# Optimization experiments

Measured on AMD Instinct MI355X. Metric: run time of the kernel, lower is better.

Reference implementation:

```python
import jax, jax.numpy as jnp
import numpy as np

T, B, S = 32, 128, 64          # decode steps, batch, source length
H = 1024                        # hidden size
EW, EF = 512, 64                # word / field embedding sizes
VW, VF = 32000, 512             # word / field vocab sizes
L = 2                           # GRU layers


def setup_inputs() -> dict:
    key = jax.random.key(0)
    ks = jax.random.split(key, 24)
    s = 0.02
    return {
        "word_ids": jax.random.randint(ks[0], (T, B), 0, VW),
        "field_ids": jax.random.randint(ks[1], (T, B), 0, VF),
        "lengths": jnp.full((B,), S, dtype=jnp.int32),  # unused in forward math
        "hidden": jax.random.normal(ks[2], (L, B, H), jnp.float32) * s,
        "context": jax.random.normal(ks[3], (B, S, H), jnp.float32),
        "context_mask": jnp.ones((B, S), dtype=bool),
        "prev_output": jnp.zeros((B, H), jnp.float32),
        "word_emb_table": jax.random.normal(ks[4], (VW, EW), jnp.float32) * s,
        "field_emb_table": jax.random.normal(ks[5], (VF, EF), jnp.float32) * s,
        "gru0_Wih": jax.random.normal(ks[6], (3 * H, EW + EF + H), jnp.float32) * s,
        "gru0_Whh": jax.random.normal(ks[7], (3 * H, H), jnp.float32) * s,
        "gru0_bih": jnp.zeros((3 * H,), jnp.float32),
        "gru0_bhh": jnp.zeros((3 * H,), jnp.float32),
        "gru1_Wih": jax.random.normal(ks[8], (3 * H, H), jnp.float32) * s,
        "gru1_Whh": jax.random.normal(ks[9], (3 * H, H), jnp.float32) * s,
        "gru1_bih": jnp.zeros((3 * H,), jnp.float32),
        "gru1_bhh": jnp.zeros((3 * H,), jnp.float32),
        "attn_Wa": jax.random.normal(ks[10], (H, H), jnp.float32) * s,
        "attn_Wc": jax.random.normal(ks[11], (H, 2 * H), jnp.float32) * s,
        "gen_Ww": jax.random.normal(ks[12], (VW, H), jnp.float32) * s,
        "gen_bw": jnp.zeros((VW,), jnp.float32),
        "gen_Wf": jax.random.normal(ks[13], (VF, H), jnp.float32) * s,
        "gen_bf": jnp.zeros((VF,), jnp.float32),
    }


def _gru_cell(x, h, Wih, Whh, bih, bhh):
    # torch.nn.GRUCell math
    gi = x @ Wih.T + bih      # (B, 3H)
    gh = h @ Whh.T + bhh
    i_r, i_z, i_n = jnp.split(gi, 3, axis=-1)
    h_r, h_z, h_n = jnp.split(gh, 3, axis=-1)
    r = jax.nn.sigmoid(i_r + h_r)
    z = jax.nn.sigmoid(i_z + h_z)
    n = jnp.tanh(i_n + r * h_n)
    return (1.0 - z) * n + z * h


def _forward(word_ids, field_ids, hidden, context, context_mask, prev_output,
             word_emb_table, field_emb_table,
             gru0_Wih, gru0_Whh, gru0_bih, gru0_bhh,
             gru1_Wih, gru1_Whh, gru1_bih, gru1_bhh,
             attn_Wa, attn_Wc, gen_Ww, gen_bw, gen_Wf, gen_bf):
    w_emb = jnp.take(word_emb_table, word_ids, axis=0)    # (T, B, EW)
    f_emb = jnp.take(field_emb_table, field_ids, axis=0)  # (T, B, EF)

    def step(carry, emb):
        hid, out = carry
        we, fe = emb
        x = jnp.concatenate([we, fe, out], axis=-1)        # input feeding
        h0 = _gru_cell(x, hid[0], gru0_Wih, gru0_Whh, gru0_bih, gru0_bhh)
        h1 = _gru_cell(h0, hid[1], gru1_Wih, gru1_Whh, gru1_bih, gru1_bhh)
        new_hid = jnp.stack([h0, h1])
        # global attention, 'general' alignment
        q = h1 @ attn_Wa.T                                  # (B, H)
        scores = jnp.einsum('bh,bsh->bs', q, context)       # (B, S)
        scores = jnp.where(context_mask, scores, -1e9)
        attn = jax.nn.softmax(scores, axis=-1)
        ctx = jnp.einsum('bs,bsh->bh', attn, context)       # (B, H)
        out = jnp.tanh(jnp.concatenate([ctx, h1], axis=-1) @ attn_Wc.T)
        # generator: word + field scores
        ws = out @ gen_Ww.T + gen_bw                        # (B, VW)
        fs = out @ gen_Wf.T + gen_bf                        # (B, VF)
        return (new_hid, out), (ws, fs)

    (hidden, output), (word_scores, field_scores) = jax.lax.scan(
        step, (hidden, prev_output), (w_emb, f_emb))
    return word_scores, field_scores, hidden, output


def reference(word_ids, field_ids, lengths, hidden, context, context_mask,
              prev_output, word_emb_table, field_emb_table,
              gru0_Wih, gru0_Whh, gru0_bih, gru0_bhh,
              gru1_Wih, gru1_Whh, gru1_bih, gru1_bhh,
              attn_Wa, attn_Wc, gen_Ww, gen_bw, gen_Wf, gen_bf):
    return _forward(word_ids, field_ids, hidden, context, context_mask,
                    prev_output, word_emb_table, field_emb_table,
                    gru0_Wih, gru0_Whh, gru0_bih, gru0_bhh,
                    gru1_Wih, gru1_Whh, gru1_bih, gru1_bhh,
                    attn_Wa, attn_Wc, gen_Ww, gen_bw, gen_Wf, gen_bf)
```

## Files before the change

### kernel.cpp

```cpp
#include <hip/hip_runtime.h>


using u16 = unsigned short;
typedef __attribute__((ext_vector_type(4))) float f32x4;
typedef __attribute__((ext_vector_type(4))) u16 u16x4;
typedef __attribute__((ext_vector_type(8))) u16 u16x8;
typedef __attribute__((ext_vector_type(8))) __bf16 bf16x8;

#define DEVFN static __device__ __forceinline__

DEVFN u16 f2bf(float f) {
  unsigned u = __float_as_uint(f);
  return (u16)((u + 0x7FFFu + ((u >> 16) & 1u)) >> 16);
}
DEVFN float bf2f(u16 h) { return __uint_as_float(((unsigned)h) << 16); }
DEVFN float sigm(float x) { return 1.0f / (1.0f + expf(-x)); }
DEVFN float gru_gate(float ir, float iz, float inn,
                     float hr, float hz, float hn, float hprev) {
  float r = sigm(ir + hr);
  float z = sigm(iz + hz);
  float n = tanhf(inn + r * hn);
  return (1.0f - z) * n + z * hprev;
}

struct GemmB3 {
  const u16* A[3];
  const u16* B[3];
  void* C[3];
  int ldb[3];
};

template <int BM, int BN, int OUTMODE, bool BIAS>
__global__ __launch_bounds__(256) void gemm_bt(
    GemmB3 args, int lda, int ldc, int Mtiles, int K,
    const float* __restrict__ bias, int swz) {
  constexpr int MF = BM / 32;
  constexpr int NF = BN / 32;
  constexpr int IA = (BM * 8) / 256;
  constexpr int IB = (BN * 8) / 256;
  __shared__ alignas(16) u16 lsA[BM * 64];
  __shared__ alignas(16) u16 lsB[BN * 64];

  const int g = blockIdx.y;
  int bx = blockIdx.x;
  if (swz) bx = (bx & 7) * ((int)gridDim.x >> 3) + (bx >> 3);
  const int nt = bx / Mtiles;
  const int mt = bx - nt * Mtiles;
  const int tid = threadIdx.x;
  const int lane = tid & 63;
  const int wv = tid >> 6;
  const int wr = wv >> 1, wc = wv & 1;
  const int l15 = lane & 15, l4 = lane >> 4;
  const int ldb = args.ldb[g];
  const u16* __restrict__ Ag = args.A[g] + (size_t)mt * BM * lda;
  const u16* __restrict__ Bg = args.B[g] + (size_t)nt * BN * ldb;

  f32x4 acc[MF][NF];
#pragma unroll
  for (int m = 0; m < MF; ++m)
#pragma unroll
    for (int n = 0; n < NF; ++n) acc[m][n] = f32x4{0.f, 0.f, 0.f, 0.f};

  const int KT = K >> 6;
  for (int kt = 0; kt < KT; ++kt) {
#pragma unroll
    for (int i = 0; i < IA; ++i) {
      const int chunk = i * 256 + tid;
      const int row = chunk >> 3, c8 = chunk & 7;
      const int cs = c8 ^ (row & 7);
      u16x8 v = *reinterpret_cast<const u16x8*>(
          Ag + (size_t)row * lda + (kt * 64 + c8 * 8));
      *reinterpret_cast<u16x8*>(lsA + row * 64 + cs * 8) = v;
    }
#pragma unroll
    for (int i = 0; i < IB; ++i) {
      const int chunk = i * 256 + tid;
      const int row = chunk >> 3, c8 = chunk & 7;
      const int cs = c8 ^ (row & 7);
      u16x8 v = *reinterpret_cast<const u16x8*>(
          Bg + (size_t)row * ldb + (kt * 64 + c8 * 8));
      *reinterpret_cast<u16x8*>(lsB + row * 64 + cs * 8) = v;
    }
    __syncthreads();
#pragma unroll
    for (int ks = 0; ks < 2; ++ks) {
      bf16x8 av[MF], bv[NF];
#pragma unroll
      for (int m = 0; m < MF; ++m) {
        const int row = wr * (BM / 2) + m * 16 + l15;
        const int cc = (ks * 4 + l4) ^ (row & 7);
        av[m] = *reinterpret_cast<const bf16x8*>(lsA + row * 64 + cc * 8);
      }
#pragma unroll
      for (int n = 0; n < NF; ++n) {
        const int row = wc * (BN / 2) + n * 16 + l15;
        const int cc = (ks * 4 + l4) ^ (row & 7);
        bv[n] = *reinterpret_cast<const bf16x8*>(lsB + row * 64 + cc * 8);
      }
#pragma unroll
      for (int m = 0; m < MF; ++m)
#pragma unroll
        for (int n = 0; n < NF; ++n)
          acc[m][n] = __builtin_amdgcn_mfma_f32_16x16x32_bf16(
              av[m], bv[n], acc[m][n], 0, 0, 0);
    }
    __syncthreads();
  }

#pragma unroll
  for (int m = 0; m < MF; ++m) {
    const int grow = mt * BM + wr * (BM / 2) + m * 16 + l4 * 4;
#pragma unroll
    for (int n = 0; n < NF; ++n) {
      const int gcol = nt * BN + wc * (BN / 2) + n * 16 + l15;
      const float bsv = BIAS ? bias[gcol] : 0.f;
#pragma unroll
      for (int j = 0; j < 4; ++j) {
        const float v = acc[m][n][j] + bsv;
        const size_t idx = (size_t)(grow + j) * ldc + gcol;
        if constexpr (OUTMODE == 0) {
          ((float*)args.C[g])[idx] = v;
        } else {
          ((u16*)args.C[g])[idx] = f2bf(v);
        }
      }
    }
  }
}

struct GemmP {
  const u16* A[3];
  const u16* B[3];
};

template <int BM, int BN>
__global__ __launch_bounds__(256) void gemm_part(
    GemmP args, int lda, int ldb, int N, int Ntiles, int KS, int nkt,
    int Mrows, float* __restrict__ Cpart) {
  constexpr int MF = BM / 32;
  constexpr int NF = BN / 32;
  constexpr int IA = (BM * 8) / 256;
  constexpr int IB = (BN * 8) / 256;
  __shared__ alignas(16) u16 lsA[BM * 64];
  __shared__ alignas(16) u16 lsB[BN * 64];

  const int g = blockIdx.y;
  const int bx = blockIdx.x;
  const int tile = bx / KS;
  const int ks = bx - tile * KS;
  const int mt = tile / Ntiles;
  const int nt = tile - mt * Ntiles;
  const int tid = threadIdx.x;
  const int lane = tid & 63;
  const int wv = tid >> 6;
  const int wr = wv >> 1, wc = wv & 1;
  const int l15 = lane & 15, l4 = lane >> 4;
  const u16* __restrict__ Ag = args.A[g] + (size_t)mt * BM * lda;
  const u16* __restrict__ Bg = args.B[g] + (size_t)nt * BN * ldb;
  float* __restrict__ Cg =
      Cpart + (size_t)(g * KS + ks) * Mrows * N + (size_t)mt * BM * N;

  f32x4 acc[MF][NF];
#pragma unroll
  for (int m = 0; m < MF; ++m)
#pragma unroll
    for (int n = 0; n < NF; ++n) acc[m][n] = f32x4{0.f, 0.f, 0.f, 0.f};

  const int kt0 = ks * nkt;
  for (int kk = 0; kk < nkt; ++kk) {
    const int kt = kt0 + kk;
#pragma unroll
    for (int i = 0; i < IA; ++i) {
      const int chunk = i * 256 + tid;
      const int row = chunk >> 3, c8 = chunk & 7;
      const int cs = c8 ^ (row & 7);
      u16x8 v = *reinterpret_cast<const u16x8*>(
          Ag + (size_t)row * lda + (kt * 64 + c8 * 8));
      *reinterpret_cast<u16x8*>(lsA + row * 64 + cs * 8) = v;
    }
#pragma unroll
    for (int i = 0; i < IB; ++i) {
      const int chunk = i * 256 + tid;
      const int row = chunk >> 3, c8 = chunk & 7;
      const int cs = c8 ^ (row & 7);
      u16x8 v = *reinterpret_cast<const u16x8*>(
          Bg + (size_t)row * ldb + (kt * 64 + c8 * 8));
      *reinterpret_cast<u16x8*>(lsB + row * 64 + cs * 8) = v;
    }
    __syncthreads();
#pragma unroll
    for (int k2 = 0; k2 < 2; ++k2) {
      bf16x8 av[MF], bv[NF];
#pragma unroll
      for (int m = 0; m < MF; ++m) {
        const int row = wr * (BM / 2) + m * 16 + l15;
        const int cc = (k2 * 4 + l4) ^ (row & 7);
        av[m] = *reinterpret_cast<const bf16x8*>(lsA + row * 64 + cc * 8);
      }
#pragma unroll
      for (int n = 0; n < NF; ++n) {
        const int row = wc * (BN / 2) + n * 16 + l15;
        const int cc = (k2 * 4 + l4) ^ (row & 7);
        bv[n] = *reinterpret_cast<const bf16x8*>(lsB + row * 64 + cc * 8);
      }
#pragma unroll
      for (int m = 0; m < MF; ++m)
#pragma unroll
        for (int n = 0; n < NF; ++n)
          acc[m][n] = __builtin_amdgcn_mfma_f32_16x16x32_bf16(
              av[m], bv[n], acc[m][n], 0, 0, 0);
    }
    __syncthreads();
  }

#pragma unroll
  for (int m = 0; m < MF; ++m) {
    const int row = wr * (BM / 2) + m * 16 + l4 * 4;
#pragma unroll
    for (int n = 0; n < NF; ++n) {
      const int col = nt * BN + wc * (BN / 2) + n * 16 + l15;
#pragma unroll
      for (int j = 0; j < 4; ++j)
        Cg[(size_t)(row + j) * N + col] = acc[m][n][j];
    }
  }
}

__global__ __launch_bounds__(256) void cvt_bf16_vec(
    const float* __restrict__ in, u16* __restrict__ out, int n4) {
  int i = blockIdx.x * 256 + threadIdx.x;
  const int stride = gridDim.x * 256;
  for (; i < n4; i += stride) {
    f32x4 v = ((const f32x4*)in)[i];
    u16x4 o;
    o[0] = f2bf(v[0]); o[1] = f2bf(v[1]); o[2] = f2bf(v[2]); o[3] = f2bf(v[3]);
    ((u16x4*)out)[i] = o;
  }
}

__global__ __launch_bounds__(256) void split3_w4(
    const float* __restrict__ W0ih, const float* __restrict__ W0hh,
    const float* __restrict__ W1ih, const float* __restrict__ W1hh,
    u16* __restrict__ W0ihO3, u16* __restrict__ W0hh3,
    u16* __restrict__ W1ih3, u16* __restrict__ W1hh3) {
  const int g = blockIdx.y;
  const int idx = blockIdx.x * 256 + threadIdx.x;
  const int r = idx >> 10, c = idx & 1023;
  const float* src;
  int ld, ofs;
  u16* dst;
  if (g == 0) { src = W0ih; ld = 1600; ofs = 576; dst = W0ihO3; }
  else if (g == 1) { src = W0hh; ld = 1024; ofs = 0; dst = W0hh3; }
  else if (g == 2) { src = W1ih; ld = 1024; ofs = 0; dst = W1ih3; }
  else { src = W1hh; ld = 1024; ofs = 0; dst = W1hh3; }
  const float x = src[(size_t)r * ld + ofs + c];
  const u16 hi = f2bf(x);
  const u16 lo = f2bf(x - bf2f(hi));
  u16* d = dst + (size_t)r * 3072;
  d[c] = hi;
  d[1024 + c] = hi;
  d[2048 + c] = lo;
}

template <bool BSIDE>
__global__ __launch_bounds__(256) void split3(
    const float* __restrict__ src, int src_ld, int src_ofs,
    u16* __restrict__ dst, int C, int total) {
  const int idx = blockIdx.x * 256 + threadIdx.x;
  if (idx >= total) return;
  const int r = idx / C, c = idx - r * C;
  const float x = src[(size_t)r * src_ld + src_ofs + c];
  const u16 hi = f2bf(x);
  const u16 lo = f2bf(x - bf2f(hi));
  u16* d = dst + (size_t)r * (3 * C);
  d[c] = hi;
  d[C + c] = BSIDE ? hi : lo;
  d[2 * C + c] = BSIDE ? lo : hi;
}

__global__ __launch_bounds__(256) void transpose_split3(
    const float* __restrict__ Wa, u16* __restrict__ dst) {
  const int idx = blockIdx.x * 256 + threadIdx.x;
  const int i = idx >> 10, j = idx & 1023;
  const float x = Wa[idx];
  const u16 hi = f2bf(x);
  const u16 lo = f2bf(x - bf2f(hi));
  u16* d = dst + (size_t)j * 3072;
  d[i] = hi;
  d[1024 + i] = hi;
  d[2048 + i] = lo;
}

__global__ __launch_bounds__(256) void gather_emb(
    const int* __restrict__ wid, const int* __restrict__ fid,
    const float* __restrict__ wtab, const float* __restrict__ ftab,
    u16* __restrict__ Xwf) {
  const int r = blockIdx.x;
  const int w = wid[r], f = fid[r];
  u16* dst = Xwf + (size_t)r * 576;
  const float* wsrc = wtab + (size_t)w * 512;
  const float* fsrc = ftab + (size_t)f * 64;
  for (int c = threadIdx.x; c < 512; c += 256) dst[c] = f2bf(wsrc[c]);
  if (threadIdx.x < 64) dst[512 + threadIdx.x] = f2bf(fsrc[threadIdx.x]);
}

DEVFN void trip_store(u16* base3, int c, float x) {
  const u16 hi = f2bf(x);
  const u16 lo = f2bf(x - bf2f(hi));
  base3[c] = hi;
  base3[1024 + c] = lo;
  base3[2048 + c] = hi;
}

__global__ __launch_bounds__(256) void init_state(
    const float* __restrict__ hidden, const float* __restrict__ prev_out,
    float* __restrict__ h0f, float* __restrict__ h1f,
    u16* __restrict__ h0a3, u16* __restrict__ h1a3, u16* __restrict__ out3) {
  const int i = blockIdx.x * 256 + threadIdx.x;
  const int b = i >> 10, c = i & 1023;
  const float aa = hidden[i], bb = hidden[131072 + i], po = prev_out[i];
  h0f[i] = aa;
  h1f[i] = bb;
  trip_store(h0a3 + (size_t)b * 3072, c, aa);
  trip_store(h1a3 + (size_t)b * 3072, c, bb);
  trip_store(out3 + (size_t)b * 3072, c, po);
}

__global__ __launch_bounds__(256) void gate0_red(
    const float* __restrict__ Ppart, const u16* __restrict__ gi0_t,
    const float* __restrict__ bhh0, float* __restrict__ h0f,
    u16* __restrict__ h0a3) {
  const int i = blockIdx.x * 256 + threadIdx.x;
  const int b = i >> 10, c = i & 1023;
  const size_t r3 = (size_t)b * 3072;
  float pr = 0.f, pz = 0.f, pn = 0.f, qr = 0.f, qz = 0.f, qn = 0.f;
#pragma unroll
  for (int ks = 0; ks < 6; ++ks) {
    const float* P0 = Ppart + (size_t)ks * 393216 + r3;
    const float* P1 = Ppart + (size_t)(6 + ks) * 393216 + r3;
    pr += P0[c]; pz += P0[1024 + c]; pn += P0[2048 + c];
    qr += P1[c]; qz += P1[1024 + c]; qn += P1[2048 + c];
  }
  const u16* gi = gi0_t + r3;
  const float h0 = gru_gate(bf2f(gi[c]) + pr, bf2f(gi[1024 + c]) + pz,
                            bf2f(gi[2048 + c]) + pn, qr + bhh0[c],
                            qz + bhh0[1024 + c], qn + bhh0[2048 + c], h0f[i]);
  h0f[i] = h0;
  const u16 hb = f2bf(h0);
  const u16 lb = f2bf(h0 - bf2f(hb));
  h0a3[r3 + c] = hb;
  h0a3[r3 + 1024 + c] = lb;
  h0a3[r3 + 2048 + c] = hb;
}

__global__ __launch_bounds__(256) void attn_red(
    const float* __restrict__ G1ip, const float* __restrict__ Ppart,
    const float* __restrict__ bih1, const float* __restrict__ bhh1,
    const float* __restrict__ ctxWa, const float* __restrict__ ctxf,
    float* __restrict__ h1f, u16* __restrict__ h1a3, u16* __restrict__ cat3) {
  __shared__ float sh1[1024];
  __shared__ float red[256];
  __shared__ float ssc[64];
  const int b = blockIdx.x;
  const int tid = threadIdx.x;
  const int k = tid * 4;
  const size_t r3 = (size_t)b * 3072;
  const size_t r1 = (size_t)b * 1024;
  u16* catr = cat3 + (size_t)b * 6144;

  {
    f32x4 ir = {0.f, 0.f, 0.f, 0.f}, iz = ir, in_ = ir;
    f32x4 hr = ir, hz = ir, hn = ir;
#pragma unroll
    for (int ks = 0; ks < 12; ++ks) {
      const float* gi = G1ip + (size_t)ks * 393216 + r3;
      ir += *(const f32x4*)(gi + k);
      iz += *(const f32x4*)(gi + 1024 + k);
      in_ += *(const f32x4*)(gi + 2048 + k);
    }
#pragma unroll
    for (int ks = 0; ks < 6; ++ks) {
      const float* gh = Ppart + (size_t)(12 + ks) * 393216 + r3;
      hr += *(const f32x4*)(gh + k);
      hz += *(const f32x4*)(gh + 1024 + k);
      hn += *(const f32x4*)(gh + 2048 + k);
    }
    f32x4 bir = *(const f32x4*)(bih1 + k);
    f32x4 biz = *(const f32x4*)(bih1 + 1024 + k);
    f32x4 bin_ = *(const f32x4*)(bih1 + 2048 + k);
    f32x4 bhr = *(const f32x4*)(bhh1 + k);
    f32x4 bhz = *(const f32x4*)(bhh1 + 1024 + k);
    f32x4 bhn = *(const f32x4*)(bhh1 + 2048 + k);
    f32x4 hp = *(const f32x4*)(h1f + r1 + k);
    f32x4 hnew;
    u16x4 hb, lb;
#pragma unroll
    for (int j = 0; j < 4; ++j) {
      hnew[j] = gru_gate(ir[j] + bir[j], iz[j] + biz[j], in_[j] + bin_[j],
                         hr[j] + bhr[j], hz[j] + bhz[j], hn[j] + bhn[j], hp[j]);
      sh1[k + j] = hnew[j];
      hb[j] = f2bf(hnew[j]);
      lb[j] = f2bf(hnew[j] - bf2f(hb[j]));
    }
    *(f32x4*)(h1f + r1 + k) = hnew;
    *(u16x4*)(h1a3 + r3 + k) = hb;
    *(u16x4*)(h1a3 + r3 + 1024 + k) = lb;
    *(u16x4*)(h1a3 + r3 + 2048 + k) = hb;
    *(u16x4*)(catr + 1024 + k) = hb;
    *(u16x4*)(catr + 2048 + 1024 + k) = lb;
    *(u16x4*)(catr + 4096 + 1024 + k) = hb;
  }
  __syncthreads();

  const int s = tid >> 2, part = tid & 3;
  {
    const float* cw = ctxWa + ((size_t)b * 64 + s) * 1024 + part * 256;
    const float* hh = sh1 + part * 256;
    float p = 0.f;
    for (int i = 0; i < 256; i += 4) {
      f32x4 v = *(const f32x4*)(cw + i);
      p += v[0] * hh[i] + v[1] * hh[i + 1] + v[2] * hh[i + 2] +
           v[3] * hh[i + 3];
    }
    red[tid] = p;
  }
  __syncthreads();
  if (part == 0) ssc[s] = red[tid] + red[tid + 1] + red[tid + 2] + red[tid + 3];
  __syncthreads();
  if (tid == 0) {
    float mx = -1e30f;
    for (int i = 0; i < 64; ++i) mx = fmaxf(mx, ssc[i]);
    float sm = 0.f;
    for (int i = 0; i < 64; ++i) {
      float e = expf(ssc[i] - mx);
      ssc[i] = e;
      sm += e;
    }
    const float inv = 1.0f / sm;
    for (int i = 0; i < 64; ++i) ssc[i] *= inv;
  }
  __syncthreads();
  {
    float a0 = 0.f, a1 = 0.f, a2 = 0.f, a3 = 0.f;
    const float* cb = ctxf + (size_t)b * 65536 + k;
    for (int s2 = 0; s2 < 64; ++s2) {
      const float w = ssc[s2];
      f32x4 v = *(const f32x4*)(cb + (size_t)s2 * 1024);
      a0 += w * v[0]; a1 += w * v[1]; a2 += w * v[2]; a3 += w * v[3];
    }
    f32x4 cv{a0, a1, a2, a3};
    u16x4 ch, cl;
#pragma unroll
    for (int j = 0; j < 4; ++j) {
      ch[j] = f2bf(cv[j]);
      cl[j] = f2bf(cv[j] - bf2f(ch[j]));
    }
    *(u16x4*)(catr + k) = ch;
    *(u16x4*)(catr + 2048 + k) = cl;
    *(u16x4*)(catr + 4096 + k) = ch;
  }
}

__global__ __launch_bounds__(256) void out_red(
    const float* __restrict__ Wcpart, float* __restrict__ outf,
    u16* __restrict__ outall_t, u16* __restrict__ out3) {
  const int i = blockIdx.x * 256 + threadIdx.x;
  const int b = i >> 10, c = i & 1023;
  float v = 0.f;
#pragma unroll
  for (int ks = 0; ks < 16; ++ks) v += Wcpart[(size_t)ks * 131072 + i];
  const float o = tanhf(v);
  outf[i] = o;
  outall_t[i] = f2bf(o);
  const u16 hb = f2bf(o);
  const u16 lb = f2bf(o - bf2f(hb));
  u16* d = out3 + (size_t)b * 3072;
  d[c] = hb;
  d[1024 + c] = lb;
  d[2048 + c] = hb;
}

__global__ __launch_bounds__(256) void final_copy(
    const float* __restrict__ h0f, const float* __restrict__ h1f,
    const float* __restrict__ outf, float* __restrict__ dst) {
  const int i = blockIdx.x * 256 + threadIdx.x;
  if (i < 131072) dst[i] = h0f[i];
  else if (i < 262144) dst[i] = h1f[i - 131072];
  else if (i < 393216) dst[i] = outf[i - 262144];
}

extern "C" void kernel_launch(void* const* d_in, const int* in_sizes, int n_in,
                              void* d_out, int out_size, void* d_ws,
                              size_t ws_size, hipStream_t stream) {
  (void)in_sizes; (void)n_in; (void)out_size; (void)ws_size;
  const int* word_ids = (const int*)d_in[0];
  const int* field_ids = (const int*)d_in[1];
  const float* hidden = (const float*)d_in[3];
  const float* context = (const float*)d_in[4];
  const float* prev_output = (const float*)d_in[6];
  const float* wtab = (const float*)d_in[7];
  const float* ftab = (const float*)d_in[8];
  const float* W0ih = (const float*)d_in[9];
  const float* W0hh = (const float*)d_in[10];
  const float* b0ih = (const float*)d_in[11];
  const float* b0hh = (const float*)d_in[12];
  const float* W1ih = (const float*)d_in[13];
  const float* W1hh = (const float*)d_in[14];
  const float* b1ih = (const float*)d_in[15];
  const float* b1hh = (const float*)d_in[16];
  const float* Wa = (const float*)d_in[17];
  const float* Wc = (const float*)d_in[18];
  const float* Ww = (const float*)d_in[19];
  const float* bw = (const float*)d_in[20];
  const float* Wf = (const float*)d_in[21];
  const float* bfb = (const float*)d_in[22];

  char* p = (char*)d_ws;
  auto take = [&](size_t bytes) {
    char* r = p;
    p += (bytes + 255) & ~(size_t)255;
    return r;
  };
  u16* W0ih_b = (u16*)take(3072ull * 1600 * 2);
  u16* W0ihO3 = (u16*)take(3072ull * 3072 * 2);
  u16* W0hh3 = (u16*)take(3072ull * 3072 * 2);
  u16* W1ih3 = (u16*)take(3072ull * 3072 * 2);
  u16* W1hh3 = (u16*)take(3072ull * 3072 * 2);
  u16* WaT3 = (u16*)take(1024ull * 3072 * 2);
  u16* Wc3 = (u16*)take(1024ull * 6144 * 2);
  u16* Ww_b = (u16*)take(32000ull * 1024 * 2);
  u16* Wf_b = (u16*)take(512ull * 1024 * 2);
  u16* ctx3 = (u16*)take(8192ull * 3072 * 2);
  float* ctxWa_f = (float*)take(8192ull * 1024 * 4);
  u16* Xwf_b = (u16*)take(4096ull * 576 * 2);
  u16* gi0_all_b = (u16*)take(4096ull * 3072 * 2);
  u16* outall_b = (u16*)take(32ull * 128 * 1024 * 2);
  u16* out3 = (u16*)take(128ull * 3072 * 2);
  float* h0f = (float*)take(128ull * 1024 * 4);
  float* h1f = (float*)take(128ull * 1024 * 4);
  float* outf = (float*)take(128ull * 1024 * 4);
  u16* h0a3 = (u16*)take(128ull * 3072 * 2);
  u16* h1a3 = (u16*)take(128ull * 3072 * 2);
  u16* cat3 = (u16*)take(128ull * 6144 * 2);
  float* Ppart = (float*)take(18ull * 128 * 3072 * 4);
  float* G1ip = (float*)take(12ull * 128 * 3072 * 4);
  float* Wcpart = (float*)take(16ull * 128 * 1024 * 4);

  cvt_bf16_vec<<<dim3(2048), 256, 0, stream>>>(W0ih, W0ih_b, 4915200 / 4);
  split3_w4<<<dim3(12288, 4), 256, 0, stream>>>(W0ih, W0hh, W1ih, W1hh,
                                                W0ihO3, W0hh3, W1ih3, W1hh3);
  split3<true><<<dim3(8192), 256, 0, stream>>>(Wc, 2048, 0, Wc3, 2048,
                                               2097152);
  split3<false><<<dim3(32768), 256, 0, stream>>>(context, 1024, 0, ctx3, 1024,
                                                 8388608);
  transpose_split3<<<dim3(4096), 256, 0, stream>>>(Wa, WaT3);
  cvt_bf16_vec<<<dim3(2048), 256, 0, stream>>>(Ww, Ww_b, 32768000 / 4);
  cvt_bf16_vec<<<dim3(2048), 256, 0, stream>>>(Wf, Wf_b, 524288 / 4);
  gather_emb<<<dim3(4096), 256, 0, stream>>>(word_ids, field_ids, wtab, ftab,
                                             Xwf_b);
  init_state<<<dim3(512), 256, 0, stream>>>(hidden, prev_output, h0f, h1f,
                                            h0a3, h1a3, out3);

  {
    GemmB3 a{};
    a.A[0] = Xwf_b; a.B[0] = W0ih_b; a.C[0] = gi0_all_b; a.ldb[0] = 1600;
    gemm_bt<128, 128, 1, true><<<dim3(768, 1), 256, 0, stream>>>(
        a, 576, 3072, 32, 576, b0ih, 0);
  }
  {
    GemmB3 a{};
    a.A[0] = ctx3; a.B[0] = WaT3; a.C[0] = ctxWa_f; a.ldb[0] = 3072;
    gemm_bt<128, 128, 0, false><<<dim3(512, 1), 256, 0, stream>>>(
        a, 3072, 1024, 64, 3072, nullptr, 0);
  }

  for (int t = 0; t < 32; ++t) {
    {
      GemmP a{};
      a.A[0] = out3;  a.B[0] = W0ihO3;
      a.A[1] = h0a3;  a.B[1] = W0hh3;
      a.A[2] = h1a3;  a.B[2] = W1hh3;
      gemm_part<128, 64><<<dim3(288, 3), 256, 0, stream>>>(
          a, 3072, 3072, 3072, 48, 6, 8, 128, Ppart);
    }
    gate0_red<<<dim3(512), 256, 0, stream>>>(
        Ppart, gi0_all_b + (size_t)t * 393216, b0hh, h0f, h0a3);
    {
      GemmP a{};
      a.A[0] = h0a3; a.B[0] = W1ih3;
      gemm_part<128, 64><<<dim3(576, 1), 256, 0, stream>>>(
          a, 3072, 3072, 3072, 48, 12, 4, 128, G1ip);
    }
    attn_red<<<dim3(128), 256, 0, stream>>>(G1ip, Ppart, b1ih, b1hh, ctxWa_f,
                                            context, h1f, h1a3, cat3);
    {
      GemmP a{};
      a.A[0] = cat3; a.B[0] = Wc3;
      gemm_part<64, 64><<<dim3(512, 1), 256, 0, stream>>>(
          a, 6144, 6144, 1024, 16, 16, 6, 128, Wcpart);
    }
    out_red<<<dim3(512), 256, 0, stream>>>(
        Wcpart, outf, outall_b + (size_t)t * 131072, out3);
  }

  {
    GemmB3 a{};
    a.A[0] = outall_b; a.B[0] = Ww_b; a.C[0] = d_out; a.ldb[0] = 1024;
    gemm_bt<128, 128, 0, true><<<dim3(8000, 1), 256, 0, stream>>>(
        a, 1024, 32000, 32, 1024, bw, 1);
  }
  {
    GemmB3 a{};
    a.A[0] = outall_b; a.B[0] = Wf_b;
    a.C[0] = (float*)d_out + 131072000ull; a.ldb[0] = 1024;
    gemm_bt<128, 128, 0, true><<<dim3(128, 1), 256, 0, stream>>>(
        a, 1024, 512, 32, 1024, bfb, 0);
  }
  final_copy<<<dim3(1536), 256, 0, stream>>>(
      h0f, h1f, outf, (float*)d_out + 133169152ull);
}
```

Before: 2.889 ms.

## Move layer-0 hidden GEMM into layer-1 input GEMM and add nontemporal output stores

```diff
diff --git a/kernel.cpp b/kernel.cpp
--- a/kernel.cpp
+++ b/kernel.cpp
@@ -30,7 +30,7 @@
   int ldb[3];
 };
 
-template <int BM, int BN, int OUTMODE, bool BIAS>
+template <int BM, int BN, int OUTMODE, bool BIAS, bool NTSTORE>
 __global__ __launch_bounds__(256) void gemm_bt(
     GemmB3 args, int lda, int ldc, int Mtiles, int K,
     const float* __restrict__ bias, int swz) {
@@ -119,7 +119,10 @@
         const float v = acc[m][n][j] + bsv;
         const size_t idx = (size_t)(grow + j) * ldc + gcol;
         if constexpr (OUTMODE == 0) {
-          ((float*)args.C[g])[idx] = v;
+          if constexpr (NTSTORE)
+            __builtin_nontemporal_store(v, (float*)args.C[g] + idx);
+          else
+            ((float*)args.C[g])[idx] = v;
         } else {
           ((u16*)args.C[g])[idx] = f2bf(v);
         }
@@ -131,12 +134,13 @@
 struct GemmP {
   const u16* A[3];
   const u16* B[3];
+  float* C[3];
 };
 
 template <int BM, int BN>
 __global__ __launch_bounds__(256) void gemm_part(
     GemmP args, int lda, int ldb, int N, int Ntiles, int KS, int nkt,
-    int Mrows, float* __restrict__ Cpart) {
+    int Mrows) {
   constexpr int MF = BM / 32;
   constexpr int NF = BN / 32;
   constexpr int IA = (BM * 8) / 256;
@@ -158,7 +162,7 @@
   const u16* __restrict__ Ag = args.A[g] + (size_t)mt * BM * lda;
   const u16* __restrict__ Bg = args.B[g] + (size_t)nt * BN * ldb;
   float* __restrict__ Cg =
-      Cpart + (size_t)(g * KS + ks) * Mrows * N + (size_t)mt * BM * N;
+      args.C[g] + (size_t)ks * Mrows * N + (size_t)mt * BM * N;
 
   f32x4 acc[MF][NF];
 #pragma unroll
@@ -372,15 +376,12 @@
     f32x4 ir = {0.f, 0.f, 0.f, 0.f}, iz = ir, in_ = ir;
     f32x4 hr = ir, hz = ir, hn = ir;
 #pragma unroll
-    for (int ks = 0; ks < 12; ++ks) {
+    for (int ks = 0; ks < 6; ++ks) {
       const float* gi = G1ip + (size_t)ks * 393216 + r3;
+      const float* gh = Ppart + (size_t)(12 + ks) * 393216 + r3;
       ir += *(const f32x4*)(gi + k);
       iz += *(const f32x4*)(gi + 1024 + k);
       in_ += *(const f32x4*)(gi + 2048 + k);
-    }
-#pragma unroll
-    for (int ks = 0; ks < 6; ++ks) {
-      const float* gh = Ppart + (size_t)(12 + ks) * 393216 + r3;
       hr += *(const f32x4*)(gh + k);
       hz += *(const f32x4*)(gh + 1024 + k);
       hn += *(const f32x4*)(gh + 2048 + k);
@@ -543,7 +544,7 @@
   u16* h1a3 = (u16*)take(128ull * 3072 * 2);
   u16* cat3 = (u16*)take(128ull * 6144 * 2);
   float* Ppart = (float*)take(18ull * 128 * 3072 * 4);
-  float* G1ip = (float*)take(12ull * 128 * 3072 * 4);
+  float* G1ip = (float*)take(6ull * 128 * 3072 * 4);
   float* Wcpart = (float*)take(16ull * 128 * 1024 * 4);
 
   cvt_bf16_vec<<<dim3(2048), 256, 0, stream>>>(W0ih, W0ih_b, 4915200 / 4);
@@ -564,40 +565,46 @@
   {
     GemmB3 a{};
     a.A[0] = Xwf_b; a.B[0] = W0ih_b; a.C[0] = gi0_all_b; a.ldb[0] = 1600;
-    gemm_bt<128, 128, 1, true><<<dim3(768, 1), 256, 0, stream>>>(
+    gemm_bt<128, 128, 1, true, false><<<dim3(768, 1), 256, 0, stream>>>(
         a, 576, 3072, 32, 576, b0ih, 0);
   }
   {
     GemmB3 a{};
     a.A[0] = ctx3; a.B[0] = WaT3; a.C[0] = ctxWa_f; a.ldb[0] = 3072;
-    gemm_bt<128, 128, 0, false><<<dim3(512, 1), 256, 0, stream>>>(
+    gemm_bt<128, 128, 0, false, false><<<dim3(512, 1), 256, 0, stream>>>(
         a, 3072, 1024, 64, 3072, nullptr, 0);
+  }
+  {
+    GemmP a{};
+    a.A[0] = h0a3; a.B[0] = W0hh3; a.C[0] = Ppart + 6ull * 393216;
+    gemm_part<128, 64><<<dim3(288, 1), 256, 0, stream>>>(
+        a, 3072, 3072, 3072, 48, 6, 8, 128);
   }
 
   for (int t = 0; t < 32; ++t) {
     {
       GemmP a{};
-      a.A[0] = out3;  a.B[0] = W0ihO3;
-      a.A[1] = h0a3;  a.B[1] = W0hh3;
-      a.A[2] = h1a3;  a.B[2] = W1hh3;
-      gemm_part<128, 64><<<dim3(288, 3), 256, 0, stream>>>(
-          a, 3072, 3072, 3072, 48, 6, 8, 128, Ppart);
+      a.A[0] = out3;  a.B[0] = W0ihO3; a.C[0] = Ppart;
+      a.A[1] = h1a3;  a.B[1] = W1hh3;  a.C[1] = Ppart + 12ull * 393216;
+      gemm_part<128, 64><<<dim3(288, 2), 256, 0, stream>>>(
+          a, 3072, 3072, 3072, 48, 6, 8, 128);
     }
     gate0_red<<<dim3(512), 256, 0, stream>>>(
         Ppart, gi0_all_b + (size_t)t * 393216, b0hh, h0f, h0a3);
     {
       GemmP a{};
-      a.A[0] = h0a3; a.B[0] = W1ih3;
-      gemm_part<128, 64><<<dim3(576, 1), 256, 0, stream>>>(
-          a, 3072, 3072, 3072, 48, 12, 4, 128, G1ip);
+      a.A[0] = h0a3; a.B[0] = W1ih3; a.C[0] = G1ip;
+      a.A[1] = h0a3; a.B[1] = W0hh3; a.C[1] = Ppart + 6ull * 393216;
+      gemm_part<128, 64><<<dim3(288, 2), 256, 0, stream>>>(
+          a, 3072, 3072, 3072, 48, 6, 8, 128);
     }
     attn_red<<<dim3(128), 256, 0, stream>>>(G1ip, Ppart, b1ih, b1hh, ctxWa_f,
                                             context, h1f, h1a3, cat3);
     {
       GemmP a{};
-      a.A[0] = cat3; a.B[0] = Wc3;
+      a.A[0] = cat3; a.B[0] = Wc3; a.C[0] = Wcpart;
       gemm_part<64, 64><<<dim3(512, 1), 256, 0, stream>>>(
-          a, 6144, 6144, 1024, 16, 16, 6, 128, Wcpart);
+          a, 6144, 6144, 1024, 16, 16, 6, 128);
     }
     out_red<<<dim3(512), 256, 0, stream>>>(
         Wcpart, outf, outall_b + (size_t)t * 131072, out3);
@@ -606,14 +613,14 @@
   {
     GemmB3 a{};
     a.A[0] = outall_b; a.B[0] = Ww_b; a.C[0] = d_out; a.ldb[0] = 1024;
-    gemm_bt<128, 128, 0, true><<<dim3(8000, 1), 256, 0, stream>>>(
+    gemm_bt<128, 128, 0, true, true><<<dim3(8000, 1), 256, 0, stream>>>(
         a, 1024, 32000, 32, 1024, bw, 1);
   }
   {
     GemmB3 a{};
     a.A[0] = outall_b; a.B[0] = Wf_b;
     a.C[0] = (float*)d_out + 131072000ull; a.ldb[0] = 1024;
-    gemm_bt<128, 128, 0, true><<<dim3(128, 1), 256, 0, stream>>>(
+    gemm_bt<128, 128, 0, true, true><<<dim3(128, 1), 256, 0, stream>>>(
         a, 1024, 512, 32, 1024, bfb, 0);
   }
   final_copy<<<dim3(1536), 256, 0, stream>>>(
```

Result: slower. 2.961 ms (+2.5%).
